# Optimization experiments

Measured on AMD Instinct MI355X. Metric: run time of the kernel, lower is better.

The kernel has to match this reference:

```python
import jax, jax.numpy as jnp
import numpy as np

HIDDEN = 1024

def setup_inputs() -> dict:
    key = jax.random.key(0)
    k1, k2, k3 = jax.random.split(key, 3)
    X = jax.random.normal(k1, (4, 4096, HIDDEN), dtype=jnp.float32)
    # nn.Linear(hidden, 3*hidden): weight [3h, h], bias [3h]
    W = jax.random.normal(k2, (3 * HIDDEN, HIDDEN), dtype=jnp.float32) / np.sqrt(HIDDEN)
    b = jax.random.normal(k3, (3 * HIDDEN,), dtype=jnp.float32) * 0.01
    return {"X": X, "W": W, "b": b}

def reference(X, W, b):
    h = X.shape[-1]
    QKV = jnp.einsum('bsh,oh->bso', X, W) + b  # [B,S,3h]
    Q, K, V = jnp.split(QKV, 3, axis=-1)
    scores = jnp.einsum('bqh,bkh->bqk', Q, K) / jnp.sqrt(jnp.float32(h))
    attn = jax.nn.softmax(scores, axis=-1)
    return jnp.einsum('bqk,bkh->bqh', attn, V)
```

## Files before the change

kernel.cpp:

```cpp
#include <hip/hip_runtime.h>
#include <hip/hip_bf16.h>

typedef unsigned short u16;
typedef _Float16 f16x8 __attribute__((ext_vector_type(8)));
typedef _Float16 f16x2 __attribute__((ext_vector_type(2)));
typedef float f32x4 __attribute__((ext_vector_type(4)));

#if __has_builtin(__builtin_amdgcn_exp2f)
#define EXP2F(x) __builtin_amdgcn_exp2f(x)
#else
#define EXP2F(x) exp2f(x)
#endif
#define FA_C32 0.045084220027780106f

__device__ __forceinline__ f32x4 mfma16h(f16x8 a, f16x8 b, f32x4 c) {
  return __builtin_amdgcn_mfma_f32_16x16x32_f16(a, b, c, 0, 0, 0);
}
__device__ __forceinline__ unsigned pk2h(float a, float b) {
  union { _Float16 h[2]; unsigned u; } x;
  x.h[0] = (_Float16)a; x.h[1] = (_Float16)b;
  return x.u;
}
__device__ __forceinline__ u16 h1(float a) {
  union { _Float16 h; u16 u; } x; x.h = (_Float16)a; return x.u;
}

#if __has_builtin(__builtin_amdgcn_fdot2)
__device__ __forceinline__ float fdot2_(f16x2 a, f16x2 b, float c) {
  return __builtin_amdgcn_fdot2(a, b, c, false);
}
#else
__device__ __forceinline__ float fdot2_(f16x2 a, f16x2 b, float c) {
  return c + (float)a[0] * (float)b[0] + (float)a[1] * (float)b[1];
}
#endif

typedef __attribute__((address_space(1))) const unsigned int gas_u32;
typedef __attribute__((address_space(3))) unsigned int las_u32;
__device__ __forceinline__ void gl_lds16(const u16* g, u16* l) {
  __builtin_amdgcn_global_load_lds((gas_u32*)g, (las_u32*)l, 16, 0, 0);
}

__global__ __launch_bounds__(256) void cast_f16_k(const float* __restrict__ X,
                                                  u16* __restrict__ Xf,
                                                  const float* __restrict__ W,
                                                  u16* __restrict__ Wf,
                                                  int nX8, int nTot8) {
  int i = blockIdx.x * 256 + threadIdx.x;
  if (i >= nTot8) return;
  const float4* s4;
  uint4* d4;
  if (i < nX8) {
    s4 = (const float4*)X + i * 2;
    d4 = (uint4*)Xf + i;
  } else {
    s4 = (const float4*)W + (i - nX8) * 2;
    d4 = (uint4*)Wf + (i - nX8);
  }
  float4 a = s4[0], b = s4[1];
  uint4 o;
  o.x = pk2h(a.x, a.y); o.y = pk2h(a.z, a.w);
  o.z = pk2h(b.x, b.y); o.w = pk2h(b.z, b.w);
  *d4 = o;
}

template <int K_, int EPI>
__global__ __launch_bounds__(512, 1) void gemm8p(
    const u16* __restrict__ A, const u16* __restrict__ B,
    const float* __restrict__ bias, u16* __restrict__ D0, u16* __restrict__ D1,
    u16* __restrict__ D2, float* __restrict__ Df, const int ldc,
    const size_t strA, const size_t strB, const size_t strC) {
  constexpr int NT = K_ / 64;
  static_assert(NT >= 4 && (NT % 2) == 0, "need even NT >= 4");
  __shared__ __align__(16) u16 As[2][2][128 * 64];
  __shared__ __align__(16) u16 Bs[2][2][128 * 64];
  __shared__ float lds_l[256];

  const int tid = threadIdx.x, lane = tid & 63, wid = tid >> 6;
  const int l15 = lane & 15, lhi = lane >> 4;
  const int m0 = blockIdx.x * 256, n0 = blockIdx.y * 256;
  const int wm = wid >> 2, wn = wid & 3;
  const u16* Ag = A + (size_t)blockIdx.z * strA;
  const u16* Bg = B + (size_t)blockIdx.z * strB;

  const int srow8 = lane >> 3;
  const int sblk = (lane & 7) ^ srow8;

#define STAGE_Q(BUF, G, GROW0, ST)                                        \
  gl_lds16((G) + (size_t)((GROW0) + wid * 8 + srow8) * K_ +               \
               (ST) * 64 + sblk * 8,                                      \
           (BUF) + (wid * 8) * 64)

#define BAR()                                                             \
  asm volatile("" ::: "memory");                                          \
  __builtin_amdgcn_s_barrier();                                           \
  asm volatile("" ::: "memory")

#define LGKM0()                                                           \
  asm volatile("s_waitcnt lgkmcnt(0)" ::: "memory");                      \
  __builtin_amdgcn_sched_barrier(0)

#define SB0() __builtin_amdgcn_sched_barrier(0)
#define VMC6() asm volatile("s_waitcnt vmcnt(6)" ::: "memory")
#define VMC0() asm volatile("s_waitcnt vmcnt(0)" ::: "memory")

#define RD_A(DST, PB, MH)                                                 \
  _Pragma("unroll") for (int mf = 0; mf < 4; ++mf)                        \
  _Pragma("unroll") for (int ks = 0; ks < 2; ++ks)                        \
    DST[mf][ks] = *(const f16x8*)((PB) + ((MH) * 64 + mf * 16 + l15) * 64 \
                                  + (((ks * 4 + lhi) ^ (l15 & 7)) * 8));

#define RD_B(DST, PB, BO, NH)                                             \
  _Pragma("unroll") for (int nf = 0; nf < 2; ++nf)                        \
  _Pragma("unroll") for (int ks = 0; ks < 2; ++ks)                        \
    DST[nf][ks] = *(const f16x8*)((PB) + ((BO) + (NH) * 32 + nf * 16 + l15) * 64 \
                                  + (((ks * 4 + lhi) ^ (l15 & 7)) * 8));

#define MM(AV, BV, MB, NB2)                                               \
  __builtin_amdgcn_s_setprio(1);                                          \
  _Pragma("unroll") for (int mf = 0; mf < 4; ++mf)                        \
  _Pragma("unroll") for (int nf = 0; nf < 2; ++nf)                        \
  _Pragma("unroll") for (int ks = 0; ks < 2; ++ks)                        \
    acc[(MB) * 4 + mf][(NB2) * 2 + nf] =                                  \
        mfma16h(AV[mf][ks], BV[nf][ks], acc[(MB) * 4 + mf][(NB2) * 2 + nf]); \
  __builtin_amdgcn_s_setprio(0);

#define SUMA(FR, MH8)                                                     \
  if (EPI == 1 && wn == 0) {                                              \
    _Pragma("unroll") for (int mf = 0; mf < 4; ++mf)                      \
    _Pragma("unroll") for (int ks = 0; ks < 2; ++ks) {                    \
      const f16x2* _pr = (const f16x2*)&FR[mf][ks];                       \
      _Pragma("unroll") for (int j = 0; j < 4; ++j)                       \
        lsa[MH8][mf] = fdot2_(_pr[j], ones2, lsa[MH8][mf]);               \
    }                                                                     \
  }

  f32x4 acc[8][4];
#pragma unroll
  for (int i = 0; i < 8; ++i)
#pragma unroll
    for (int j = 0; j < 4; ++j) acc[i][j] = 0.f;

  float lsa[2][4];
#pragma unroll
  for (int i = 0; i < 2; ++i)
#pragma unroll
    for (int j = 0; j < 4; ++j) lsa[i][j] = 0.f;
  const f16x2 ones2 = {(_Float16)1.0f, (_Float16)1.0f};

  const int bofs = (wn & 1) * 64;

  STAGE_Q(&As[0][0][0],    Ag, m0,       0);
  STAGE_Q(&As[0][0][4096], Ag, m0 + 64,  0);
  STAGE_Q(&As[0][1][0],    Ag, m0 + 128, 0);
  STAGE_Q(&As[0][1][4096], Ag, m0 + 192, 0);
  STAGE_Q(&Bs[0][0][0],    Bg, n0,       0);
  STAGE_Q(&Bs[0][0][4096], Bg, n0 + 64,  0);
  STAGE_Q(&Bs[0][1][0],    Bg, n0 + 128, 0);
  STAGE_Q(&Bs[0][1][4096], Bg, n0 + 192, 0);
  STAGE_Q(&As[1][0][0],    Ag, m0,       1);
  STAGE_Q(&As[1][1][0],    Ag, m0 + 128, 1);
  STAGE_Q(&Bs[1][0][0],    Bg, n0,       1);
  STAGE_Q(&Bs[1][0][4096], Bg, n0 + 64,  1);
  STAGE_Q(&Bs[1][1][0],    Bg, n0 + 128, 1);
  STAGE_Q(&Bs[1][1][4096], Bg, n0 + 192, 1);
  VMC6();
  BAR();

#pragma unroll 2
  for (int u = 0; u < NT; ++u) {
    const int d = u & 1;
    const u16* Apb = &As[d][wm][0];
    const u16* Bpb = &Bs[d][wn >> 1][0];
    f16x8 a0[4][2], a1[4][2], b0[2][2], b1[2][2];

    RD_A(a0, Apb, 0);
    RD_B(b0, Bpb, bofs, 0);
    if (u + 1 < NT) {
      STAGE_Q(&As[d ^ 1][0][4096], Ag, m0 + 64,  u + 1);
      STAGE_Q(&As[d ^ 1][1][4096], Ag, m0 + 192, u + 1);
    }
    BAR();
    LGKM0();
    MM(a0, b0, 0, 0);
    SUMA(a0, 0);
    SB0();
    BAR();

    RD_B(b1, Bpb, bofs, 1);
    if (u + 2 < NT) {
      STAGE_Q(&As[d][0][0], Ag, m0,       u + 2);
      STAGE_Q(&As[d][1][0], Ag, m0 + 128, u + 2);
    }
    BAR();
    LGKM0();
    MM(a0, b1, 0, 1);
    SB0();
    BAR();

    RD_A(a1, Apb, 1);
    if (u + 2 < NT) {
      STAGE_Q(&Bs[d][0][0],    Bg, n0,       u + 2);
      STAGE_Q(&Bs[d][0][4096], Bg, n0 + 64,  u + 2);
      STAGE_Q(&Bs[d][1][0],    Bg, n0 + 128, u + 2);
      STAGE_Q(&Bs[d][1][4096], Bg, n0 + 192, u + 2);
    }
    BAR();
    LGKM0();
    MM(a1, b1, 1, 1);
    SUMA(a1, 1);
    MM(a1, b0, 1, 0);
    SB0();
    if (u + 2 < NT) { VMC6(); }
    else if (u + 2 == NT) { VMC0(); }
    BAR();
  }
#undef STAGE_Q
#undef BAR
#undef LGKM0
#undef SB0
#undef VMC6
#undef VMC0
#undef RD_A
#undef RD_B
#undef MM
#undef SUMA

  if (EPI == 2) {
    float bv[4];
#pragma unroll
    for (int cf = 0; cf < 4; ++cf) bv[cf] = bias[n0 + wn * 64 + cf * 16 + l15];
    const int region = n0 >> 10;
    const int ncol0 = (n0 & 1023) + wn * 64;
    if (region < 2) {
      u16* dst = region ? D1 : D0;
#pragma unroll
      for (int rf = 0; rf < 8; ++rf) {
        const int m = m0 + wm * 128 + rf * 16 + lhi * 4;
#pragma unroll
        for (int r = 0; r < 4; ++r)
#pragma unroll
          for (int cf = 0; cf < 4; ++cf)
            dst[(size_t)(m + r) * 1024 + ncol0 + cf * 16 + l15] = h1(acc[rf][cf][r] + bv[cf]);
      }
    } else {
#pragma unroll
      for (int rf = 0; rf < 8; ++rf) {
        const int m = m0 + wm * 128 + rf * 16 + lhi * 4;
        const int bb = m >> 12, s = m & 4095;
#pragma unroll
        for (int cf = 0; cf < 4; ++cf) {
          const int dcol = ncol0 + cf * 16 + l15;
          uint2 v;
          v.x = pk2h(acc[rf][cf][0] + bv[cf], acc[rf][cf][1] + bv[cf]);
          v.y = pk2h(acc[rf][cf][2] + bv[cf], acc[rf][cf][3] + bv[cf]);
          *(uint2*)&D2[(size_t)(bb * 1024 + dcol) * 4096 + s] = v;
        }
      }
    }
  } else if (EPI == 0) {
#pragma unroll
    for (int rf = 0; rf < 8; ++rf) {
      const int m = m0 + wm * 128 + rf * 16 + lhi * 4;
#pragma unroll
      for (int r = 0; r < 4; ++r)
#pragma unroll
        for (int cf = 0; cf < 4; ++cf) {
          const int n = n0 + wn * 64 + cf * 16 + l15;
          float p = fminf(EXP2F(acc[rf][cf][r] * FA_C32), 60000.f);
          D0[(size_t)blockIdx.z * strC + (size_t)(m + r) * ldc + n] = h1(p);
        }
    }
  } else {
    if (wn == 0) {
#pragma unroll
      for (int mh = 0; mh < 2; ++mh)
#pragma unroll
        for (int mf = 0; mf < 4; ++mf) {
          float s = lsa[mh][mf];
          s += __shfl_xor(s, 16, 64);
          s += __shfl_xor(s, 32, 64);
          if (lhi == 0) lds_l[wm * 128 + mh * 64 + mf * 16 + l15] = s;
        }
    }
    __syncthreads();
#pragma unroll
    for (int rf = 0; rf < 8; ++rf) {
      const int m = m0 + wm * 128 + rf * 16 + lhi * 4;
#pragma unroll
      for (int r = 0; r < 4; ++r) {
        const float li = 1.0f / lds_l[wm * 128 + rf * 16 + lhi * 4 + r];
#pragma unroll
        for (int cf = 0; cf < 4; ++cf) {
          const int n = n0 + wn * 64 + cf * 16 + l15;
          Df[(size_t)blockIdx.z * strC + (size_t)(m + r) * ldc + n] = acc[rf][cf][r] * li;
        }
      }
    }
  }
}

extern "C" void kernel_launch(void* const* d_in, const int* in_sizes, int n_in,
                              void* d_out, int out_size, void* d_ws, size_t ws_size,
                              hipStream_t stream) {
  const float* X = (const float*)d_in[0];
  const float* W = (const float*)d_in[1];
  const float* b = (const float*)d_in[2];
  float* out = (float*)d_out;
  char* ws = (char*)d_ws;

  const size_t SB = (size_t)4096 * 4096 * 2;
  const size_t QB = (size_t)4096 * 1024 * 2;
  const size_t WFB = (size_t)3072 * 1024 * 2;
  int NB = 1;
  if (ws_size >= 4 * SB + WFB + 12 * QB) NB = 4;
  else if (ws_size >= 2 * SB + WFB + 12 * QB) NB = 2;

  u16* S  = (u16*)(ws);
  u16* Xf = (u16*)(ws);
  u16* Wf = (u16*)(ws + (size_t)NB * SB);
  u16* Qf = (u16*)(ws + (size_t)NB * SB + WFB);
  u16* Kf = (u16*)(ws + (size_t)NB * SB + WFB + 4 * QB);
  u16* Vt = (u16*)(ws + (size_t)NB * SB + WFB + 8 * QB);

  const int nX8 = 16777216 / 8, nTot8 = nX8 + 3145728 / 8;
  cast_f16_k<<<(nTot8 + 255) / 256, 256, 0, stream>>>(X, Xf, W, Wf, nX8, nTot8);

  gemm8p<1024, 2><<<dim3(64, 12, 1), 512, 0, stream>>>(
      Xf, Wf, b, Qf, Kf, Vt, nullptr, 0, 0, 0, 0);

  const size_t strQ = (size_t)4096 * 1024;
  const size_t strS = (size_t)4096 * 4096;
  const size_t strV = (size_t)1024 * 4096;
  for (int g = 0; g < 4; g += NB) {
    const u16* Qg = Qf + (size_t)g * strQ;
    const u16* Kg = Kf + (size_t)g * strQ;
    const u16* Vg = Vt + (size_t)g * strV;
    float* Og = out + (size_t)g * strQ;
    gemm8p<1024, 0><<<dim3(16, 16, NB), 512, 0, stream>>>(
        Qg, Kg, nullptr, S, nullptr, nullptr, nullptr, 4096, strQ, strQ, strS);
    gemm8p<4096, 1><<<dim3(16, 4, NB), 512, 0, stream>>>(
        S, Vg, nullptr, nullptr, nullptr, nullptr, Og, 1024, strS, strV, strQ);
  }
}
```

Baseline: 391.2 us.

## Restructure GEMM main loop to triple-buffered 32-wide K tiles with one barrier

Replaces the double-buffered 64-wide K-tile pipeline, which had four barriers per iteration and split A/B staging, with a three-slot ring of 32-wide K tiles. Each iteration issues one combined prefetch two tiles ahead, reads all fragments at once, runs all 32 MFMAs, and synchronizes once. Precomputed swizzled LDS offsets replace the per-read address arithmetic. The aim is to cut barrier and scheduling overhead. In exchange it doubles the loop trip count, shrinks LDS use, and has less work per barrier available to hide global load latency.

After: 483.7 us. 23.6% more time.

```diff
diff --git a/kernel.cpp b/kernel.cpp
--- a/kernel.cpp
+++ b/kernel.cpp
@@ -70,10 +70,10 @@
     const float* __restrict__ bias, u16* __restrict__ D0, u16* __restrict__ D1,
     u16* __restrict__ D2, float* __restrict__ Df, const int ldc,
     const size_t strA, const size_t strB, const size_t strC) {
-  constexpr int NT = K_ / 64;
-  static_assert(NT >= 4 && (NT % 2) == 0, "need even NT >= 4");
-  __shared__ __align__(16) u16 As[2][2][128 * 64];
-  __shared__ __align__(16) u16 Bs[2][2][128 * 64];
+  constexpr int NT = K_ / 32;
+  static_assert(NT >= 4, "need >=4 K-tiles");
+  __shared__ __align__(16) u16 As3[3][128 * 64];
+  __shared__ __align__(16) u16 Bs3[3][128 * 64];
   __shared__ float lds_l[256];
 
   const int tid = threadIdx.x, lane = tid & 63, wid = tid >> 6;
@@ -83,13 +83,17 @@
   const u16* Ag = A + (size_t)blockIdx.z * strA;
   const u16* Bg = B + (size_t)blockIdx.z * strB;
 
-  const int srow8 = lane >> 3;
-  const int sblk = (lane & 7) ^ srow8;
-
-#define STAGE_Q(BUF, G, GROW0, ST)                                        \
-  gl_lds16((G) + (size_t)((GROW0) + wid * 8 + srow8) * K_ +               \
-               (ST) * 64 + sblk * 8,                                      \
-           (BUF) + (wid * 8) * 64)
+#define STAGE_OP(BUF, G, GROW0, T)                                        \
+  {                                                                       \
+    _Pragma("unroll") for (int q_ = 0; q_ < 2; ++q_) {                    \
+      const int bp_ = wid * 16 + q_ * 8;                                  \
+      const int p_ = bp_ + (lane >> 3);                                   \
+      const int sp_ = (lane & 7) ^ (p_ & 7);                              \
+      const int r_ = p_ + 128 * (sp_ >> 2);                               \
+      gl_lds16((G) + (size_t)((GROW0) + r_) * K_ + (T) * 32 + (sp_ & 3) * 8, \
+               (BUF) + bp_ * 64);                                         \
+    }                                                                     \
+  }
 
 #define BAR()                                                             \
   asm volatile("" ::: "memory");                                          \
@@ -101,38 +105,23 @@
   __builtin_amdgcn_sched_barrier(0)
 
 #define SB0() __builtin_amdgcn_sched_barrier(0)
-#define VMC6() asm volatile("s_waitcnt vmcnt(6)" ::: "memory")
+#define VMC4() asm volatile("s_waitcnt vmcnt(4)" ::: "memory")
 #define VMC0() asm volatile("s_waitcnt vmcnt(0)" ::: "memory")
 
-#define RD_A(DST, PB, MH)                                                 \
-  _Pragma("unroll") for (int mf = 0; mf < 4; ++mf)                        \
-  _Pragma("unroll") for (int ks = 0; ks < 2; ++ks)                        \
-    DST[mf][ks] = *(const f16x8*)((PB) + ((MH) * 64 + mf * 16 + l15) * 64 \
-                                  + (((ks * 4 + lhi) ^ (l15 & 7)) * 8));
-
-#define RD_B(DST, PB, BO, NH)                                             \
-  _Pragma("unroll") for (int nf = 0; nf < 2; ++nf)                        \
-  _Pragma("unroll") for (int ks = 0; ks < 2; ++ks)                        \
-    DST[nf][ks] = *(const f16x8*)((PB) + ((BO) + (NH) * 32 + nf * 16 + l15) * 64 \
-                                  + (((ks * 4 + lhi) ^ (l15 & 7)) * 8));
-
-#define MM(AV, BV, MB, NB2)                                               \
-  __builtin_amdgcn_s_setprio(1);                                          \
-  _Pragma("unroll") for (int mf = 0; mf < 4; ++mf)                        \
-  _Pragma("unroll") for (int nf = 0; nf < 2; ++nf)                        \
-  _Pragma("unroll") for (int ks = 0; ks < 2; ++ks)                        \
-    acc[(MB) * 4 + mf][(NB2) * 2 + nf] =                                  \
-        mfma16h(AV[mf][ks], BV[nf][ks], acc[(MB) * 4 + mf][(NB2) * 2 + nf]); \
-  __builtin_amdgcn_s_setprio(0);
-
-#define SUMA(FR, MH8)                                                     \
-  if (EPI == 1 && wn == 0) {                                              \
-    _Pragma("unroll") for (int mf = 0; mf < 4; ++mf)                      \
-    _Pragma("unroll") for (int ks = 0; ks < 2; ++ks) {                    \
-      const f16x2* _pr = (const f16x2*)&FR[mf][ks];                       \
-      _Pragma("unroll") for (int j = 0; j < 4; ++j)                       \
-        lsa[MH8][mf] = fdot2_(_pr[j], ones2, lsa[MH8][mf]);               \
-    }                                                                     \
+  int offA[8], offB[4];
+#pragma unroll
+  for (int mf = 0; mf < 8; ++mf) {
+    const int r_ = wm * 128 + mf * 16 + l15;
+    const int p_ = r_ & 127;
+    const int s_ = (((r_ >> 7) << 2) + lhi) ^ (p_ & 7);
+    offA[mf] = p_ * 64 + s_ * 8;
+  }
+#pragma unroll
+  for (int nf = 0; nf < 4; ++nf) {
+    const int r_ = wn * 64 + nf * 16 + l15;
+    const int p_ = r_ & 127;
+    const int s_ = (((r_ >> 7) << 2) + lhi) ^ (p_ & 7);
+    offB[nf] = p_ * 64 + s_ * 8;
   }
 
   f32x4 acc[8][4];
@@ -148,83 +137,56 @@
     for (int j = 0; j < 4; ++j) lsa[i][j] = 0.f;
   const f16x2 ones2 = {(_Float16)1.0f, (_Float16)1.0f};
 
-  const int bofs = (wn & 1) * 64;
-
-  STAGE_Q(&As[0][0][0],    Ag, m0,       0);
-  STAGE_Q(&As[0][0][4096], Ag, m0 + 64,  0);
-  STAGE_Q(&As[0][1][0],    Ag, m0 + 128, 0);
-  STAGE_Q(&As[0][1][4096], Ag, m0 + 192, 0);
-  STAGE_Q(&Bs[0][0][0],    Bg, n0,       0);
-  STAGE_Q(&Bs[0][0][4096], Bg, n0 + 64,  0);
-  STAGE_Q(&Bs[0][1][0],    Bg, n0 + 128, 0);
-  STAGE_Q(&Bs[0][1][4096], Bg, n0 + 192, 0);
-  STAGE_Q(&As[1][0][0],    Ag, m0,       1);
-  STAGE_Q(&As[1][1][0],    Ag, m0 + 128, 1);
-  STAGE_Q(&Bs[1][0][0],    Bg, n0,       1);
-  STAGE_Q(&Bs[1][0][4096], Bg, n0 + 64,  1);
-  STAGE_Q(&Bs[1][1][0],    Bg, n0 + 128, 1);
-  STAGE_Q(&Bs[1][1][4096], Bg, n0 + 192, 1);
-  VMC6();
+  STAGE_OP(&As3[0][0], Ag, m0, 0);
+  STAGE_OP(&Bs3[0][0], Bg, n0, 0);
+  STAGE_OP(&As3[1][0], Ag, m0, 1);
+  STAGE_OP(&Bs3[1][0], Bg, n0, 1);
+  VMC4();
   BAR();
 
-#pragma unroll 2
+  int sl = 0;
   for (int u = 0; u < NT; ++u) {
-    const int d = u & 1;
-    const u16* Apb = &As[d][wm][0];
-    const u16* Bpb = &Bs[d][wn >> 1][0];
-    f16x8 a0[4][2], a1[4][2], b0[2][2], b1[2][2];
-
-    RD_A(a0, Apb, 0);
-    RD_B(b0, Bpb, bofs, 0);
-    if (u + 1 < NT) {
-      STAGE_Q(&As[d ^ 1][0][4096], Ag, m0 + 64,  u + 1);
-      STAGE_Q(&As[d ^ 1][1][4096], Ag, m0 + 192, u + 1);
-    }
-    BAR();
+    if (u + 2 < NT) {
+      const int s2 = (sl >= 1) ? sl - 1 : sl + 2;
+      STAGE_OP(&As3[s2][0], Ag, m0, u + 2);
+      STAGE_OP(&Bs3[s2][0], Bg, n0, u + 2);
+    }
+    const u16* Apb = &As3[sl][0];
+    const u16* Bpb = &Bs3[sl][0];
+    f16x8 a[8], b[4];
+#pragma unroll
+    for (int mf = 0; mf < 8; ++mf) a[mf] = *(const f16x8*)(Apb + offA[mf]);
+#pragma unroll
+    for (int nf = 0; nf < 4; ++nf) b[nf] = *(const f16x8*)(Bpb + offB[nf]);
     LGKM0();
-    MM(a0, b0, 0, 0);
-    SUMA(a0, 0);
+    __builtin_amdgcn_s_setprio(1);
+#pragma unroll
+    for (int mf = 0; mf < 8; ++mf)
+#pragma unroll
+      for (int nf = 0; nf < 4; ++nf)
+        acc[mf][nf] = mfma16h(a[mf], b[nf], acc[mf][nf]);
+    __builtin_amdgcn_s_setprio(0);
+    if (EPI == 1 && wn == 0) {
+#pragma unroll
+      for (int mf = 0; mf < 8; ++mf) {
+        const f16x2* pr = (const f16x2*)&a[mf];
+#pragma unroll
+        for (int j = 0; j < 4; ++j)
+          lsa[mf >> 2][mf & 3] = fdot2_(pr[j], ones2, lsa[mf >> 2][mf & 3]);
+      }
+    }
     SB0();
-    BAR();
-
-    RD_B(b1, Bpb, bofs, 1);
-    if (u + 2 < NT) {
-      STAGE_Q(&As[d][0][0], Ag, m0,       u + 2);
-      STAGE_Q(&As[d][1][0], Ag, m0 + 128, u + 2);
-    }
-    BAR();
-    LGKM0();
-    MM(a0, b1, 0, 1);
-    SB0();
-    BAR();
-
-    RD_A(a1, Apb, 1);
-    if (u + 2 < NT) {
-      STAGE_Q(&Bs[d][0][0],    Bg, n0,       u + 2);
-      STAGE_Q(&Bs[d][0][4096], Bg, n0 + 64,  u + 2);
-      STAGE_Q(&Bs[d][1][0],    Bg, n0 + 128, u + 2);
-      STAGE_Q(&Bs[d][1][4096], Bg, n0 + 192, u + 2);
-    }
-    BAR();
-    LGKM0();
-    MM(a1, b1, 1, 1);
-    SUMA(a1, 1);
-    MM(a1, b0, 1, 0);
-    SB0();
-    if (u + 2 < NT) { VMC6(); }
+    if (u + 2 < NT) { VMC4(); }
     else if (u + 2 == NT) { VMC0(); }
     BAR();
-  }
-#undef STAGE_Q
+    sl = (sl == 2) ? 0 : sl + 1;
+  }
+#undef STAGE_OP
 #undef BAR
 #undef LGKM0
 #undef SB0
-#undef VMC6
+#undef VMC4
 #undef VMC0
-#undef RD_A
-#undef RD_B
-#undef MM
-#undef SUMA
 
   if (EPI == 2) {
     float bv[4];
```
